# Optimization experiments

Measured on AMD Instinct MI355X. Metric: run time of the kernel, lower is better.

Reference implementation:

```python
import jax, jax.numpy as jnp
import numpy as np

DIM = 128
BATCH = 8192
# Static index sets (constants, mirror diag_ind / tril_ind / diag_ind_tril)
TRIL_R, TRIL_C = np.tril_indices(DIM)          # row/col of lower-tri entries, row-major
DIAG_IN_TRIL = np.nonzero(TRIL_R == TRIL_C)[0]  # positions of diagonal entries in flat tril vector
DIAG = np.arange(DIM)
N_TRIL = TRIL_R.size  # dim*(dim+1)/2 = 8256


def setup_inputs() -> dict:
    key = jax.random.key(0)
    x = jax.random.normal(key, (BATCH, N_TRIL), dtype=jnp.float32)
    return {"x": x}


def reference(x):
    # Scatter-fill batched lower-triangular matrix L: [..., DIM, DIM]
    batch_shape = x.shape[:-1]
    L = jnp.zeros(batch_shape + (DIM, DIM), dtype=x.dtype)
    L = L.at[..., TRIL_R, TRIL_C].set(x)
    # Overwrite diagonal with log1p(exp(x_diag) + 1e-12) (softplus-like, as in source)
    diag = jnp.log1p(jnp.exp(x[..., DIAG_IN_TRIL]) + 1e-12)
    L = L.at[..., DIAG, DIAG].set(diag)
    # Diffusion matrix L @ L^T
    return jnp.einsum('...ik,...jk->...ij', L, L)
```

## Files before the change

kernel.cpp:

```cpp
#include <hip/hip_runtime.h>
#include <math.h>


#define DIM        128
#define NTRIL      8256
#define ROW_BYTES  256
#define NB         4

typedef __bf16 bf16x8 __attribute__((ext_vector_type(8)));
typedef float  f32x16 __attribute__((ext_vector_type(16)));

struct RcTab { unsigned short off[NTRIL]; };
static constexpr RcTab make_tab() {
    RcTab t{};
    int idx = 0;
    for (int r = 0; r < DIM; ++r)
        for (int c = 0; c <= r; ++c)
            t.off[idx++] = (unsigned short)((r * ROW_BYTES + c * 2) ^ ((r & 7) << 4));
    return t;
}
__device__ const RcTab TBL = make_tab();

__device__ __forceinline__ int rowbase(int r) {
    return (r << 8) ^ ((r & 7) << 4);
}

__global__ __launch_bounds__(256) void tril2diff_kernel(
    const float* __restrict__ x, float* __restrict__ out)
{
    __shared__ alignas(16) __bf16 Lsh[DIM * ROW_BYTES / 2];

    const int tid = threadIdx.x;
    const int b0  = blockIdx.x * NB;

    ushort4 o[8], ot;
    #pragma unroll
    for (int i = 0; i < 8; ++i)
        o[i] = *(const ushort4*)(TBL.off + (tid + i * 256) * 4);
    if (tid < 16)
        ot = *(const ushort4*)(TBL.off + (2048 + tid) * 4);

    float4 v[8], vt;
    float  dvx;
    {
        const float* xb = x + (size_t)b0 * NTRIL;
        #pragma unroll
        for (int i = 0; i < 8; ++i)
            v[i] = *(const float4*)(xb + (tid + i * 256) * 4);
        if (tid < 16)
            vt = *(const float4*)(xb + (2048 + tid) * 4);
        if (tid < DIM)
            dvx = xb[(tid * (tid + 1)) / 2 + tid];
    }

    uint4* lz4 = (uint4*)Lsh;
    #pragma unroll
    for (int i = 0; i < 8; ++i)
        lz4[tid + i * 256] = uint4{0u, 0u, 0u, 0u};
    __syncthreads();

    const int lane = tid & 63;
    const int wv   = tid >> 6;
    const int i0   = (wv >> 1) * 64;
    const int j0   = (wv & 1) * 64;
    const int cl   = lane & 31;
    const int hh   = lane >> 5;
    const int kb   = hh * 16;
    const int ba0 = rowbase(i0      + cl);
    const int ba1 = rowbase(i0 + 32 + cl);
    const int bb0 = rowbase(j0      + cl);
    const int bb1 = rowbase(j0 + 32 + cl);

    char*       lbw = (char*)Lsh;
    const char* lb  = (const char*)Lsh;

    for (int n = 0; n < NB; ++n) {
        #pragma unroll
        for (int i = 0; i < 8; ++i) {
            *(__bf16*)(lbw + o[i].x) = (__bf16)v[i].x;
            *(__bf16*)(lbw + o[i].y) = (__bf16)v[i].y;
            *(__bf16*)(lbw + o[i].z) = (__bf16)v[i].z;
            *(__bf16*)(lbw + o[i].w) = (__bf16)v[i].w;
        }
        if (tid < 16) {
            *(__bf16*)(lbw + ot.x) = (__bf16)vt.x;
            *(__bf16*)(lbw + ot.y) = (__bf16)vt.y;
            *(__bf16*)(lbw + ot.z) = (__bf16)vt.z;
            *(__bf16*)(lbw + ot.w) = (__bf16)vt.w;
        }
        float dv;
        if (tid < DIM)
            dv = log1pf(expf(dvx) + 1e-12f);
        __syncthreads();

        if (tid < DIM)
            *(__bf16*)(lbw + ((tid * ROW_BYTES + tid * 2) ^ ((tid & 7) << 4))) = (__bf16)dv;
        __syncthreads();

        if (n + 1 < NB) {
            const float* xb = x + (size_t)(b0 + n + 1) * NTRIL;
            #pragma unroll
            for (int i = 0; i < 8; ++i)
                v[i] = *(const float4*)(xb + (tid + i * 256) * 4);
            if (tid < 16)
                vt = *(const float4*)(xb + (2048 + tid) * 4);
            if (tid < DIM)
                dvx = xb[(tid * (tid + 1)) / 2 + tid];
        }

        f32x16 acc00 = {0}, acc01 = {0}, acc10 = {0}, acc11 = {0};

#define MFMA_STEP(ks)                                                          \
    {                                                                          \
        const int koff = (ks) * 32 + kb;                                       \
        bf16x8 a0 = *(const bf16x8*)(lb + (ba0 ^ koff));                       \
        bf16x8 a1 = *(const bf16x8*)(lb + (ba1 ^ koff));                       \
        bf16x8 b0 = *(const bf16x8*)(lb + (bb0 ^ koff));                       \
        bf16x8 b1 = *(const bf16x8*)(lb + (bb1 ^ koff));                       \
        acc00 = __builtin_amdgcn_mfma_f32_32x32x16_bf16(a0, b0, acc00, 0, 0, 0); \
        acc01 = __builtin_amdgcn_mfma_f32_32x32x16_bf16(a0, b1, acc01, 0, 0, 0); \
        acc10 = __builtin_amdgcn_mfma_f32_32x32x16_bf16(a1, b0, acc10, 0, 0, 0); \
        acc11 = __builtin_amdgcn_mfma_f32_32x32x16_bf16(a1, b1, acc11, 0, 0, 0); \
    }

        #pragma unroll
        for (int ks = 0; ks < 4; ++ks)
            MFMA_STEP(ks);
        if (wv == 3) {
            #pragma unroll
            for (int ks = 4; ks < 8; ++ks)
                MFMA_STEP(ks);
        }
#undef MFMA_STEP

        __syncthreads();

        float* ob = out + (size_t)(b0 + n) * (DIM * DIM);
        #pragma unroll
        for (int reg = 0; reg < 16; ++reg) {
            const int row = (reg & 3) + 8 * (reg >> 2) + 4 * hh;
            ob[(i0      + row) * DIM + j0      + cl] = acc00[reg];
            ob[(i0      + row) * DIM + j0 + 32 + cl] = acc01[reg];
            ob[(i0 + 32 + row) * DIM + j0      + cl] = acc10[reg];
            ob[(i0 + 32 + row) * DIM + j0 + 32 + cl] = acc11[reg];
        }
    }
}

extern "C" void kernel_launch(void* const* d_in, const int* in_sizes, int n_in,
                              void* d_out, int out_size, void* d_ws, size_t ws_size,
                              hipStream_t stream) {
    const float* x = (const float*)d_in[0];
    float* out = (float*)d_out;
    const int batch = in_sizes[0] / NTRIL;
    tril2diff_kernel<<<batch / NB, 256, 0, stream>>>(x, out);
}
```

Baseline: 683.6 us.

## Skip zero K-blocks per 32x32 tile, fuse diagonal softplus into scatter, halve NB

Each 32x32 MFMA sub-tile now runs only as many K-steps as its triangular extent requires, using per-wave template limits. This cuts redundant MFMAs and LDS reads over the zero upper triangle. The diagonal softplus is folded into the scatter through a flag bit in the offset table, which removes one barrier and the separate diagonal load. The per-block batch count drops from 4 to 2, doubling the grid while shortening each block's serial chain.

```diff
diff --git a/kernel.cpp b/kernel.cpp
--- a/kernel.cpp
+++ b/kernel.cpp
@@ -5,7 +5,7 @@
 #define DIM        128
 #define NTRIL      8256
 #define ROW_BYTES  256
-#define NB         4
+#define NB         2
 
 typedef __bf16 bf16x8 __attribute__((ext_vector_type(8)));
 typedef float  f32x16 __attribute__((ext_vector_type(16)));
@@ -15,14 +15,50 @@
     RcTab t{};
     int idx = 0;
     for (int r = 0; r < DIM; ++r)
-        for (int c = 0; c <= r; ++c)
-            t.off[idx++] = (unsigned short)((r * ROW_BYTES + c * 2) ^ ((r & 7) << 4));
+        for (int c = 0; c <= r; ++c) {
+            unsigned short o = (unsigned short)((r * ROW_BYTES + c * 2) ^ ((r & 7) << 4));
+            if (c == r) o |= 0x8000;
+            t.off[idx++] = o;
+        }
     return t;
 }
 __device__ const RcTab TBL = make_tab();
 
 __device__ __forceinline__ int rowbase(int r) {
     return (r << 8) ^ ((r & 7) << 4);
+}
+
+#define SCAT1(oo, vv)                                                \
+    {                                                                \
+        float f = (vv);                                              \
+        const unsigned short u = (oo);                               \
+        if (__builtin_expect((u & 0x8000u) != 0, 0))                 \
+            f = log1pf(expf(f) + 1e-12f);                            \
+        *(__bf16*)(lbw + (u & 0x7fffu)) = (__bf16)f;                 \
+    }
+
+template<int L00, int L01, int L10, int L11>
+__device__ __forceinline__ void mfma_quad(
+    const char* lb, int ba0, int ba1, int bb0, int bb1, int kb,
+    f32x16& acc00, f32x16& acc01, f32x16& acc10, f32x16& acc11)
+{
+    constexpr int LA0 = (L00 > L01) ? L00 : L01;
+    constexpr int LA1 = (L10 > L11) ? L10 : L11;
+    constexpr int LB0 = (L00 > L10) ? L00 : L10;
+    constexpr int LB1 = (L01 > L11) ? L01 : L11;
+    #pragma unroll
+    for (int ks = 0; ks < 8; ++ks) {
+        const int koff = ks * 32 + kb;
+        bf16x8 a0{}, a1{}, b0{}, b1{};
+        if (ks < LA0) a0 = *(const bf16x8*)(lb + (ba0 ^ koff));
+        if (ks < LA1) a1 = *(const bf16x8*)(lb + (ba1 ^ koff));
+        if (ks < LB0) b0 = *(const bf16x8*)(lb + (bb0 ^ koff));
+        if (ks < LB1) b1 = *(const bf16x8*)(lb + (bb1 ^ koff));
+        if (ks < L00) acc00 = __builtin_amdgcn_mfma_f32_32x32x16_bf16(a0, b0, acc00, 0, 0, 0);
+        if (ks < L01) acc01 = __builtin_amdgcn_mfma_f32_32x32x16_bf16(a0, b1, acc01, 0, 0, 0);
+        if (ks < L10) acc10 = __builtin_amdgcn_mfma_f32_32x32x16_bf16(a1, b0, acc10, 0, 0, 0);
+        if (ks < L11) acc11 = __builtin_amdgcn_mfma_f32_32x32x16_bf16(a1, b1, acc11, 0, 0, 0);
+    }
 }
 
 __global__ __launch_bounds__(256) void tril2diff_kernel(
@@ -41,7 +77,6 @@
         ot = *(const ushort4*)(TBL.off + (2048 + tid) * 4);
 
     float4 v[8], vt;
-    float  dvx;
     {
         const float* xb = x + (size_t)b0 * NTRIL;
         #pragma unroll
@@ -49,8 +84,6 @@
             v[i] = *(const float4*)(xb + (tid + i * 256) * 4);
         if (tid < 16)
             vt = *(const float4*)(xb + (2048 + tid) * 4);
-        if (tid < DIM)
-            dvx = xb[(tid * (tid + 1)) / 2 + tid];
     }
 
     uint4* lz4 = (uint4*)Lsh;
@@ -77,24 +110,17 @@
     for (int n = 0; n < NB; ++n) {
         #pragma unroll
         for (int i = 0; i < 8; ++i) {
-            *(__bf16*)(lbw + o[i].x) = (__bf16)v[i].x;
-            *(__bf16*)(lbw + o[i].y) = (__bf16)v[i].y;
-            *(__bf16*)(lbw + o[i].z) = (__bf16)v[i].z;
-            *(__bf16*)(lbw + o[i].w) = (__bf16)v[i].w;
+            SCAT1(o[i].x, v[i].x);
+            SCAT1(o[i].y, v[i].y);
+            SCAT1(o[i].z, v[i].z);
+            SCAT1(o[i].w, v[i].w);
         }
         if (tid < 16) {
-            *(__bf16*)(lbw + ot.x) = (__bf16)vt.x;
-            *(__bf16*)(lbw + ot.y) = (__bf16)vt.y;
-            *(__bf16*)(lbw + ot.z) = (__bf16)vt.z;
-            *(__bf16*)(lbw + ot.w) = (__bf16)vt.w;
+            SCAT1(ot.x, vt.x);
+            SCAT1(ot.y, vt.y);
+            SCAT1(ot.z, vt.z);
+            SCAT1(ot.w, vt.w);
         }
-        float dv;
-        if (tid < DIM)
-            dv = log1pf(expf(dvx) + 1e-12f);
-        __syncthreads();
-
-        if (tid < DIM)
-            *(__bf16*)(lbw + ((tid * ROW_BYTES + tid * 2) ^ ((tid & 7) << 4))) = (__bf16)dv;
         __syncthreads();
 
         if (n + 1 < NB) {
@@ -104,34 +130,23 @@
                 v[i] = *(const float4*)(xb + (tid + i * 256) * 4);
             if (tid < 16)
                 vt = *(const float4*)(xb + (2048 + tid) * 4);
-            if (tid < DIM)
-                dvx = xb[(tid * (tid + 1)) / 2 + tid];
         }
 
         f32x16 acc00 = {0}, acc01 = {0}, acc10 = {0}, acc11 = {0};
-
-#define MFMA_STEP(ks)                                                          \
-    {                                                                          \
-        const int koff = (ks) * 32 + kb;                                       \
-        bf16x8 a0 = *(const bf16x8*)(lb + (ba0 ^ koff));                       \
-        bf16x8 a1 = *(const bf16x8*)(lb + (ba1 ^ koff));                       \
-        bf16x8 b0 = *(const bf16x8*)(lb + (bb0 ^ koff));                       \
-        bf16x8 b1 = *(const bf16x8*)(lb + (bb1 ^ koff));                       \
-        acc00 = __builtin_amdgcn_mfma_f32_32x32x16_bf16(a0, b0, acc00, 0, 0, 0); \
-        acc01 = __builtin_amdgcn_mfma_f32_32x32x16_bf16(a0, b1, acc01, 0, 0, 0); \
-        acc10 = __builtin_amdgcn_mfma_f32_32x32x16_bf16(a1, b0, acc10, 0, 0, 0); \
-        acc11 = __builtin_amdgcn_mfma_f32_32x32x16_bf16(a1, b1, acc11, 0, 0, 0); \
-    }
-
-        #pragma unroll
-        for (int ks = 0; ks < 4; ++ks)
-            MFMA_STEP(ks);
-        if (wv == 3) {
-            #pragma unroll
-            for (int ks = 4; ks < 8; ++ks)
-                MFMA_STEP(ks);
+        switch (wv) {
+        case 0:
+            mfma_quad<2, 2, 2, 4>(lb, ba0, ba1, bb0, bb1, kb, acc00, acc01, acc10, acc11);
+            break;
+        case 1:
+            mfma_quad<2, 2, 4, 4>(lb, ba0, ba1, bb0, bb1, kb, acc00, acc01, acc10, acc11);
+            break;
+        case 2:
+            mfma_quad<2, 4, 2, 4>(lb, ba0, ba1, bb0, bb1, kb, acc00, acc01, acc10, acc11);
+            break;
+        default:
+            mfma_quad<6, 6, 6, 8>(lb, ba0, ba1, bb0, bb1, kb, acc00, acc01, acc10, acc11);
+            break;
         }
-#undef MFMA_STEP
 
         __syncthreads();
 
```

New measurement: 851.6 us. 24.6% more time.
